# Kernel optimization log

Measured on AMD Instinct MI355X. Metric: run time of the kernel, lower is better.

The kernel has to match this reference:

```python
import jax, jax.numpy as jnp
import numpy as np

B, T, D_MODEL, N_HEADS = 2, 2048, 4096, 32
D_HEAD = D_MODEL // N_HEADS
ROPE_THETA = 20000.0


def _rope_tables(seq_len, d_head, theta):
    # Faithful to RotaryEmbedding + apply_rotary_emb's `[..., ::2]` slicing:
    # emb = concat(freqs, freqs) along feature dim, then every-other element taken.
    inv_freq = 1.0 / (theta ** (jnp.arange(0, d_head, 2, dtype=jnp.float32) / d_head))  # [d/2]
    t = jnp.arange(seq_len, dtype=jnp.float32)
    freqs = jnp.einsum('i,j->ij', t, inv_freq)          # [T, d/2]
    emb = jnp.concatenate([freqs, freqs], axis=-1)       # [T, d]
    cos_h = jnp.cos(emb)[:, ::2]                         # [T, d/2]
    sin_h = jnp.sin(emb)[:, ::2]                         # [T, d/2]
    return cos_h, sin_h


def _apply_rope(x, cos_h, sin_h):
    # x: [B, H, T, d]; pairs are interleaved (even/odd feature indices).
    x1 = x[..., 0::2]
    x2 = x[..., 1::2]
    r1 = x1 * cos_h - x2 * sin_h
    r2 = x1 * sin_h + x2 * cos_h
    return jnp.stack((r1, r2), axis=-1).reshape(x.shape)


def setup_inputs() -> dict:
    key = jax.random.key(0)
    kx, kq, kk, kv, ko = jax.random.split(key, 5)
    s = 0.02
    return {
        'hidden_states': jax.random.normal(kx, (B, T, D_MODEL), dtype=jnp.float32),
        'Wq': jax.random.normal(kq, (D_MODEL, D_MODEL), dtype=jnp.float32) * s,
        'Wk': jax.random.normal(kk, (D_MODEL, D_MODEL), dtype=jnp.float32) * s,
        'Wv': jax.random.normal(kv, (D_MODEL, D_MODEL), dtype=jnp.float32) * s,
        'Wo': jax.random.normal(ko, (D_MODEL, D_MODEL), dtype=jnp.float32) * s,
    }


def reference(hidden_states, Wq, Wk, Wv, Wo):
    Bs, Ts, C = hidden_states.shape
    H, Dh = N_HEADS, C // N_HEADS

    # QKV projections (nn.Linear: y = x @ W.T), split heads -> [B, H, T, Dh]
    def proj(W):
        return (hidden_states @ W.T).reshape(Bs, Ts, H, Dh).transpose(0, 2, 1, 3)

    q, k, v = proj(Wq), proj(Wk), proj(Wv)

    cos_h, sin_h = _rope_tables(Ts, Dh, ROPE_THETA)
    q = _apply_rope(q, cos_h, sin_h)
    k = _apply_rope(k, cos_h, sin_h)

    # Causal scaled-dot-product attention (flash path semantics)
    scale = 1.0 / jnp.sqrt(jnp.asarray(Dh, dtype=q.dtype))
    scores = jnp.einsum('bhqd,bhkd->bhqk', q, k) * scale      # [B,H,T,T]
    causal = jnp.tril(jnp.ones((Ts, Ts), dtype=bool))
    scores = jnp.where(causal, scores, jnp.finfo(scores.dtype).min)
    probs = jax.nn.softmax(scores, axis=-1)
    attn = jnp.einsum('bhqk,bhkd->bhqd', probs, v)            # [B,H,T,Dh]

    attn = attn.transpose(0, 2, 1, 3).reshape(Bs, Ts, C)
    return attn @ Wo.T
```

## Files before the change

### kernel.cpp

```cpp
#include <hip/hip_runtime.h>
#include <hip/hip_bf16.h>


typedef __bf16 bf16x8 __attribute__((ext_vector_type(8)));
typedef __bf16 bf16x4 __attribute__((ext_vector_type(4)));
typedef float  f32x4  __attribute__((ext_vector_type(4)));

#define GLD_A1(p) ((__attribute__((address_space(1))) void*)(p))
#define GLD_A3(p) ((__attribute__((address_space(3))) void*)(p))

static constexpr int   BATCH = 2;
static constexpr int   TSEQ  = 2048;
static constexpr int   DM    = 4096;
static constexpr int   NH    = 32;
static constexpr int   DH    = 128;
static constexpr size_t TS   = (size_t)DM * DM;

__global__ __launch_bounds__(256) void cast_f32_bf16(const float* __restrict__ in,
                                                     __bf16* __restrict__ out) {
    size_t id = (size_t)blockIdx.x * blockDim.x + threadIdx.x;
    float4 v = ((const float4*)in)[id];
    bf16x4 o = { (__bf16)v.x, (__bf16)v.y, (__bf16)v.z, (__bf16)v.w };
    *(bf16x4*)(out + id * 4) = o;
}

template <bool OUT_F32>
__global__ __launch_bounds__(256) void gemm_nt(const __bf16* __restrict__ A,
                                               const __bf16* __restrict__ W,
                                               void* __restrict__ Cout) {
    constexpr int Kd = 4096, Nd = 4096;
    __shared__ alignas(16) __bf16 As[128 * 32];
    __shared__ alignas(16) __bf16 Bs[128 * 32];

    const int t = threadIdx.x, w = t >> 6, L = t & 63;
    const int lane15 = L & 15, quad = L >> 4;
    const int rowBlock = blockIdx.y * 128, colBlock = blockIdx.x * 128;
    const int wr = (w >> 1) * 64, wc = (w & 1) * 64;

    f32x4 acc[4][4] = {};

    for (int kb = 0; kb < Kd; kb += 32) {
        __syncthreads();
#pragma unroll
        for (int i = 0; i < 2; i++) {
            const int chunk = w * 128 + i * 64 + L;
            const int row = chunk >> 2, c8 = (chunk & 3) * 8;
            __builtin_amdgcn_global_load_lds(
                GLD_A1(A + (size_t)(rowBlock + row) * Kd + kb + c8),
                GLD_A3(As + (size_t)(w * 128 + i * 64) * 8), 16, 0, 0);
            __builtin_amdgcn_global_load_lds(
                GLD_A1(W + (size_t)(colBlock + row) * Kd + kb + c8),
                GLD_A3(Bs + (size_t)(w * 128 + i * 64) * 8), 16, 0, 0);
        }
        __syncthreads();

        bf16x8 a[4], b[4];
#pragma unroll
        for (int i = 0; i < 4; i++)
            a[i] = *(const bf16x8*)(As + (wr + i * 16 + lane15) * 32 + quad * 8);
#pragma unroll
        for (int j = 0; j < 4; j++)
            b[j] = *(const bf16x8*)(Bs + (wc + j * 16 + lane15) * 32 + quad * 8);
#pragma unroll
        for (int i = 0; i < 4; i++)
#pragma unroll
            for (int j = 0; j < 4; j++)
                acc[i][j] = __builtin_amdgcn_mfma_f32_16x16x32_bf16(a[i], b[j], acc[i][j], 0, 0, 0);
    }

#pragma unroll
    for (int i = 0; i < 4; i++)
#pragma unroll
        for (int j = 0; j < 4; j++)
#pragma unroll
            for (int r = 0; r < 4; r++) {
                const size_t gm = rowBlock + wr + i * 16 + quad * 4 + r;
                const size_t gn = colBlock + wc + j * 16 + lane15;
                if (OUT_F32)
                    ((float*)Cout)[gm * Nd + gn] = acc[i][j][r];
                else
                    ((__bf16*)Cout)[gm * Nd + gn] = (__bf16)acc[i][j][r];
            }
}

__global__ __launch_bounds__(256) void rope_inplace(__bf16* __restrict__ X) {
    const size_t id = (size_t)blockIdx.x * blockDim.x + threadIdx.x;
    const int g = (int)(id & 511);
    const size_t row = id >> 9;
    const int tpos = (int)(row & (TSEQ - 1));
    __bf16* p = X + row * DM + (size_t)g * 8;
    bf16x8 v = *(const bf16x8*)p;
    bf16x8 o;
#pragma unroll
    for (int pr = 0; pr < 4; pr++) {
        const int pcol = g * 4 + pr;
        const int j = (2 * (pcol & 63)) & 63;
        const float inv = exp2f(-(float)j * (14.287712379549449f / 64.0f));
        const float ang = (float)tpos * inv;
        float s, c;
        sincosf(ang, &s, &c);
        const float x0 = (float)v[2 * pr], x1 = (float)v[2 * pr + 1];
        o[2 * pr]     = (__bf16)(x0 * c - x1 * s);
        o[2 * pr + 1] = (__bf16)(x0 * s + x1 * c);
    }
    *(bf16x8*)p = o;
}

__global__ __launch_bounds__(256) void flash_attn(const __bf16* __restrict__ Qg,
                                                  const __bf16* __restrict__ Kg,
                                                  const __bf16* __restrict__ Vg,
                                                  __bf16* __restrict__ Og) {
    const int qb = blockIdx.x;
    const int bh = blockIdx.y;
    const int b = bh >> 5, h = bh & 31;
    const size_t base = (size_t)b * TSEQ * DM + (size_t)h * DH;
    const __bf16* Qp = Qg + base;
    const __bf16* Kp = Kg + base;
    const __bf16* Vp = Vg + base;
    __bf16*       Op = Og + base;

    __shared__ alignas(16) __bf16 Ks[64 * 128];
    __shared__ alignas(16) __bf16 Vt[128 * 64];
    __shared__ alignas(16) __bf16 Ps[64 * 72];

    const int t = threadIdx.x, w = t >> 6, L = t & 63;
    const int lane15 = L & 15, quad = L >> 4;
    const int sw = (lane15 & 7) << 4;

    bf16x8 aq[4];
    {
        const int qrow = qb * 64 + w * 16 + lane15;
#pragma unroll
        for (int ks = 0; ks < 4; ++ks)
            aq[ks] = *(const bf16x8*)(Qp + (size_t)qrow * DM + ks * 32 + quad * 8);
    }

    f32x4 o[8] = {};
    float m_i[4], l_i[4];
#pragma unroll
    for (int r = 0; r < 4; r++) { m_i[r] = -1e30f; l_i[r] = 0.0f; }
    const float scale = 0.08838834764831845f;

    for (int kt = 0; kt <= qb; ++kt) {
        bf16x8 vv[4];
#pragma unroll
        for (int c = 0; c < 4; c++) {
            const int d0 = (c * 4 + w) * 8;
            vv[c] = *(const bf16x8*)(Vp + (size_t)(kt * 64 + L) * DM + d0);
        }
#pragma unroll
        for (int c = 0; c < 4; c++) {
            const int chunk0 = c * 256 + (w << 6);
            const int chunk  = chunk0 + L;
            const int row = chunk >> 4;
            const int ssw = (chunk & 15) ^ (row & 7);
            __builtin_amdgcn_global_load_lds(
                GLD_A1(Kp + (size_t)(kt * 64 + row) * DM + ssw * 8),
                GLD_A3((char*)Ks + chunk0 * 16), 16, 0, 0);
        }
#pragma unroll
        for (int c = 0; c < 4; c++) {
            const int d0 = (c * 4 + w) * 8;
#pragma unroll
            for (int jj = 0; jj < 8; jj++)
                *(__bf16*)((char*)Vt + (d0 + jj) * 128 + ((L * 2) ^ (jj << 4))) = vv[c][jj];
        }
        __syncthreads();

        f32x4 s[4] = {};
        __builtin_amdgcn_s_setprio(1);
#pragma unroll
        for (int ks = 0; ks < 4; ++ks)
#pragma unroll
            for (int n = 0; n < 4; n++) {
                bf16x8 bk = *(const bf16x8*)((const char*)Ks + (n * 16 + lane15) * 256
                                             + ((ks * 64 + quad * 16) ^ sw));
                s[n] = __builtin_amdgcn_mfma_f32_16x16x32_bf16(aq[ks], bk, s[n], 0, 0, 0);
            }
        __builtin_amdgcn_s_setprio(0);

        const bool diag = (kt == qb);
#pragma unroll
        for (int n = 0; n < 4; n++) {
            const int col = kt * 64 + n * 16 + lane15;
#pragma unroll
            for (int r = 0; r < 4; r++) {
                const int rowq = qb * 64 + w * 16 + quad * 4 + r;
                float sv = s[n][r] * scale;
                if (diag && col > rowq) sv = -1e30f;
                s[n][r] = sv;
            }
        }

        float mx[4], al[4], rs[4];
#pragma unroll
        for (int r = 0; r < 4; r++)
            mx[r] = fmaxf(fmaxf(s[0][r], s[1][r]), fmaxf(s[2][r], s[3][r]));
#pragma unroll
        for (int off = 8; off >= 1; off >>= 1)
#pragma unroll
            for (int r = 0; r < 4; r++)
                mx[r] = fmaxf(mx[r], __shfl_xor(mx[r], off));
#pragma unroll
        for (int r = 0; r < 4; r++) {
            const float mn = fmaxf(m_i[r], mx[r]);
            al[r] = __expf(m_i[r] - mn);
            m_i[r] = mn;
            rs[r] = 0.0f;
        }
#pragma unroll
        for (int n = 0; n < 4; n++)
#pragma unroll
            for (int r = 0; r < 4; r++) {
                const float p = __expf(s[n][r] - m_i[r]);
                rs[r] += p;
                Ps[(w * 16 + quad * 4 + r) * 72 + n * 16 + lane15] = (__bf16)p;
            }
#pragma unroll
        for (int off = 8; off >= 1; off >>= 1)
#pragma unroll
            for (int r = 0; r < 4; r++)
                rs[r] += __shfl_xor(rs[r], off);
#pragma unroll
        for (int r = 0; r < 4; r++) l_i[r] = l_i[r] * al[r] + rs[r];
#pragma unroll
        for (int d = 0; d < 8; ++d)
#pragma unroll
            for (int r = 0; r < 4; r++) o[d][r] *= al[r];

        __syncthreads();

        __builtin_amdgcn_s_setprio(1);
#pragma unroll
        for (int ks2 = 0; ks2 < 2; ++ks2) {
            bf16x8 ap = *(const bf16x8*)(Ps + (w * 16 + lane15) * 72 + ks2 * 32 + quad * 8);
#pragma unroll
            for (int d = 0; d < 8; ++d) {
                bf16x8 bv = *(const bf16x8*)((const char*)Vt + (d * 16 + lane15) * 128
                                             + ((ks2 * 64 + quad * 16) ^ sw));
                o[d] = __builtin_amdgcn_mfma_f32_16x16x32_bf16(ap, bv, o[d], 0, 0, 0);
            }
        }
        __builtin_amdgcn_s_setprio(0);
        __syncthreads();
    }

    float inv_l[4];
#pragma unroll
    for (int r = 0; r < 4; r++) inv_l[r] = 1.0f / l_i[r];
#pragma unroll
    for (int d = 0; d < 8; ++d)
#pragma unroll
        for (int r = 0; r < 4; r++) {
            const int rowq = qb * 64 + w * 16 + quad * 4 + r;
            Op[(size_t)rowq * DM + d * 16 + lane15] = (__bf16)(o[d][r] * inv_l[r]);
        }
}

extern "C" void kernel_launch(void* const* d_in, const int* in_sizes, int n_in,
                              void* d_out, int out_size, void* d_ws, size_t ws_size,
                              hipStream_t stream) {
    const float* hs = (const float*)d_in[0];
    const float* Wq = (const float*)d_in[1];
    const float* Wk = (const float*)d_in[2];
    const float* Wv = (const float*)d_in[3];
    const float* Wo = (const float*)d_in[4];
    float* out = (float*)d_out;

    __bf16* hs_b = (__bf16*)d_ws;
    __bf16* wq_b = hs_b + TS;
    __bf16* wk_b = wq_b + TS;
    __bf16* wv_b = wk_b + TS;
    __bf16* wo_b = wv_b + TS;
    __bf16* Qb   = wo_b + TS;
    __bf16* Kb   = Qb + TS;
    __bf16* Vb   = Kb + TS;
    __bf16* Ab   = Vb + TS;
    if (ws_size < 9 * TS * sizeof(__bf16)) return;

    const dim3 blk(256);
    const int castGrid = (int)(TS / 4 / 256);
    cast_f32_bf16<<<castGrid, blk, 0, stream>>>(hs, hs_b);
    cast_f32_bf16<<<castGrid, blk, 0, stream>>>(Wq, wq_b);
    cast_f32_bf16<<<castGrid, blk, 0, stream>>>(Wk, wk_b);
    cast_f32_bf16<<<castGrid, blk, 0, stream>>>(Wv, wv_b);
    cast_f32_bf16<<<castGrid, blk, 0, stream>>>(Wo, wo_b);

    const dim3 ggrid(32, 32);
    gemm_nt<false><<<ggrid, blk, 0, stream>>>(hs_b, wq_b, (void*)Qb);
    gemm_nt<false><<<ggrid, blk, 0, stream>>>(hs_b, wk_b, (void*)Kb);
    gemm_nt<false><<<ggrid, blk, 0, stream>>>(hs_b, wv_b, (void*)Vb);

    const int ropeGrid = (int)(TS / 8 / 256);
    rope_inplace<<<ropeGrid, blk, 0, stream>>>(Qb);
    rope_inplace<<<ropeGrid, blk, 0, stream>>>(Kb);

    flash_attn<<<dim3(32, 64), blk, 0, stream>>>(Qb, Kb, Vb, Ab);

    gemm_nt<true><<<ggrid, blk, 0, stream>>>(Ab, wo_b, (void*)out);
}
```

Measured before the change: 1.507 ms.

## Prefetch next K/V tile in flash attention, reverse block order, batch cast/rope launches

The flash attention loop now double-buffers K in shared memory and issues the next tile's K and V global loads before computing on the current one, so load latency overlaps with compute. Q blocks are dispatched longest-first to reduce the causal-triangle tail. The five cast kernels and the two RoPE kernels are each merged into a single launch via a second grid dimension. The extra K buffer raises LDS use, which can lower occupancy, and the held V registers add register pressure.

```diff
diff --git a/kernel.cpp b/kernel.cpp
--- a/kernel.cpp
+++ b/kernel.cpp
@@ -16,12 +16,19 @@
 static constexpr int   DH    = 128;
 static constexpr size_t TS   = (size_t)DM * DM;
 
-__global__ __launch_bounds__(256) void cast_f32_bf16(const float* __restrict__ in,
-                                                     __bf16* __restrict__ out) {
+__global__ __launch_bounds__(256) void cast5_f32_bf16(const float* __restrict__ s0,
+                                                      const float* __restrict__ s1,
+                                                      const float* __restrict__ s2,
+                                                      const float* __restrict__ s3,
+                                                      const float* __restrict__ s4,
+                                                      __bf16* __restrict__ out) {
+    const int which = blockIdx.y;
+    const float* s = which == 0 ? s0 : which == 1 ? s1 : which == 2 ? s2
+                   : which == 3 ? s3 : s4;
     size_t id = (size_t)blockIdx.x * blockDim.x + threadIdx.x;
-    float4 v = ((const float4*)in)[id];
+    float4 v = ((const float4*)s)[id];
     bf16x4 o = { (__bf16)v.x, (__bf16)v.y, (__bf16)v.z, (__bf16)v.w };
-    *(bf16x4*)(out + id * 4) = o;
+    *(bf16x4*)(out + (size_t)which * TS + id * 4) = o;
 }
 
 template <bool OUT_F32>
@@ -83,7 +90,9 @@
             }
 }
 
-__global__ __launch_bounds__(256) void rope_inplace(__bf16* __restrict__ X) {
+__global__ __launch_bounds__(256) void rope2_inplace(__bf16* __restrict__ Q,
+                                                     __bf16* __restrict__ K) {
+    __bf16* X = blockIdx.y == 0 ? Q : K;
     const size_t id = (size_t)blockIdx.x * blockDim.x + threadIdx.x;
     const int g = (int)(id & 511);
     const size_t row = id >> 9;
@@ -110,7 +119,7 @@
                                                   const __bf16* __restrict__ Kg,
                                                   const __bf16* __restrict__ Vg,
                                                   __bf16* __restrict__ Og) {
-    const int qb = blockIdx.x;
+    const int qb = 31 - blockIdx.x;
     const int bh = blockIdx.y;
     const int b = bh >> 5, h = bh & 31;
     const size_t base = (size_t)b * TSEQ * DM + (size_t)h * DH;
@@ -119,7 +128,7 @@
     const __bf16* Vp = Vg + base;
     __bf16*       Op = Og + base;
 
-    __shared__ alignas(16) __bf16 Ks[64 * 128];
+    __shared__ alignas(16) __bf16 Ks[2][64 * 128];
     __shared__ alignas(16) __bf16 Vt[128 * 64];
     __shared__ alignas(16) __bf16 Ps[64 * 72];
 
@@ -141,12 +150,12 @@
     for (int r = 0; r < 4; r++) { m_i[r] = -1e30f; l_i[r] = 0.0f; }
     const float scale = 0.08838834764831845f;
 
-    for (int kt = 0; kt <= qb; ++kt) {
-        bf16x8 vv[4];
+    {
+        bf16x8 v0[4];
 #pragma unroll
         for (int c = 0; c < 4; c++) {
             const int d0 = (c * 4 + w) * 8;
-            vv[c] = *(const bf16x8*)(Vp + (size_t)(kt * 64 + L) * DM + d0);
+            v0[c] = *(const bf16x8*)(Vp + (size_t)L * DM + d0);
         }
 #pragma unroll
         for (int c = 0; c < 4; c++) {
@@ -155,17 +164,42 @@
             const int row = chunk >> 4;
             const int ssw = (chunk & 15) ^ (row & 7);
             __builtin_amdgcn_global_load_lds(
-                GLD_A1(Kp + (size_t)(kt * 64 + row) * DM + ssw * 8),
-                GLD_A3((char*)Ks + chunk0 * 16), 16, 0, 0);
+                GLD_A1(Kp + (size_t)row * DM + ssw * 8),
+                GLD_A3((char*)Ks[0] + chunk0 * 16), 16, 0, 0);
         }
 #pragma unroll
         for (int c = 0; c < 4; c++) {
             const int d0 = (c * 4 + w) * 8;
 #pragma unroll
             for (int jj = 0; jj < 8; jj++)
-                *(__bf16*)((char*)Vt + (d0 + jj) * 128 + ((L * 2) ^ (jj << 4))) = vv[c][jj];
-        }
-        __syncthreads();
+                *(__bf16*)((char*)Vt + (d0 + jj) * 128 + ((L * 2) ^ (jj << 4))) = v0[c][jj];
+        }
+    }
+    __syncthreads();
+
+    int cur = 0;
+    for (int kt = 0; kt <= qb; ++kt) {
+        const int nxt = cur ^ 1;
+        const bool pf = (kt < qb);
+
+        bf16x8 vv[4];
+        if (pf) {
+#pragma unroll
+            for (int c = 0; c < 4; c++) {
+                const int d0 = (c * 4 + w) * 8;
+                vv[c] = *(const bf16x8*)(Vp + (size_t)((kt + 1) * 64 + L) * DM + d0);
+            }
+#pragma unroll
+            for (int c = 0; c < 4; c++) {
+                const int chunk0 = c * 256 + (w << 6);
+                const int chunk  = chunk0 + L;
+                const int row = chunk >> 4;
+                const int ssw = (chunk & 15) ^ (row & 7);
+                __builtin_amdgcn_global_load_lds(
+                    GLD_A1(Kp + (size_t)((kt + 1) * 64 + row) * DM + ssw * 8),
+                    GLD_A3((char*)Ks[nxt] + chunk0 * 16), 16, 0, 0);
+            }
+        }
 
         f32x4 s[4] = {};
         __builtin_amdgcn_s_setprio(1);
@@ -173,7 +207,7 @@
         for (int ks = 0; ks < 4; ++ks)
 #pragma unroll
             for (int n = 0; n < 4; n++) {
-                bf16x8 bk = *(const bf16x8*)((const char*)Ks + (n * 16 + lane15) * 256
+                bf16x8 bk = *(const bf16x8*)((const char*)Ks[cur] + (n * 16 + lane15) * 256
                                              + ((ks * 64 + quad * 16) ^ sw));
                 s[n] = __builtin_amdgcn_mfma_f32_16x16x32_bf16(aq[ks], bk, s[n], 0, 0, 0);
             }
@@ -228,7 +262,7 @@
 #pragma unroll
             for (int r = 0; r < 4; r++) o[d][r] *= al[r];
 
-        __syncthreads();
+        asm volatile("s_waitcnt lgkmcnt(0)\n\ts_barrier" ::: "memory");
 
         __builtin_amdgcn_s_setprio(1);
 #pragma unroll
@@ -242,7 +276,20 @@
             }
         }
         __builtin_amdgcn_s_setprio(0);
+
+        asm volatile("s_waitcnt lgkmcnt(0)\n\ts_barrier" ::: "memory");
+
+        if (pf) {
+#pragma unroll
+            for (int c = 0; c < 4; c++) {
+                const int d0 = (c * 4 + w) * 8;
+#pragma unroll
+                for (int jj = 0; jj < 8; jj++)
+                    *(__bf16*)((char*)Vt + (d0 + jj) * 128 + ((L * 2) ^ (jj << 4))) = vv[c][jj];
+            }
+        }
         __syncthreads();
+        cur = nxt;
     }
 
     float inv_l[4];
@@ -279,21 +326,14 @@
     if (ws_size < 9 * TS * sizeof(__bf16)) return;
 
     const dim3 blk(256);
-    const int castGrid = (int)(TS / 4 / 256);
-    cast_f32_bf16<<<castGrid, blk, 0, stream>>>(hs, hs_b);
-    cast_f32_bf16<<<castGrid, blk, 0, stream>>>(Wq, wq_b);
-    cast_f32_bf16<<<castGrid, blk, 0, stream>>>(Wk, wk_b);
-    cast_f32_bf16<<<castGrid, blk, 0, stream>>>(Wv, wv_b);
-    cast_f32_bf16<<<castGrid, blk, 0, stream>>>(Wo, wo_b);
+    cast5_f32_bf16<<<dim3(TS / 4 / 256, 5), blk, 0, stream>>>(hs, Wq, Wk, Wv, Wo, hs_b);
 
     const dim3 ggrid(32, 32);
     gemm_nt<false><<<ggrid, blk, 0, stream>>>(hs_b, wq_b, (void*)Qb);
     gemm_nt<false><<<ggrid, blk, 0, stream>>>(hs_b, wk_b, (void*)Kb);
     gemm_nt<false><<<ggrid, blk, 0, stream>>>(hs_b, wv_b, (void*)Vb);
 
-    const int ropeGrid = (int)(TS / 8 / 256);
-    rope_inplace<<<ropeGrid, blk, 0, stream>>>(Qb);
-    rope_inplace<<<ropeGrid, blk, 0, stream>>>(Kb);
+    rope2_inplace<<<dim3(TS / 8 / 256, 2), blk, 0, stream>>>(Qb, Kb);
 
     flash_attn<<<dim3(32, 64), blk, 0, stream>>>(Qb, Kb, Vb, Ab);
 
```

Result: no change. 1.487 ms (-1.3%).
